# Kernel optimization log

Measured on AMD Instinct MI355X. Metric: run time of the kernel, lower is better.

The kernel has to match this reference:

```python
import jax, jax.numpy as jnp
import numpy as np

R = 65  # num_relations


def rgcn_conv(x, edge_index, edge_type, W, root, bias):
    """PyG RGCNConv with per-relation mean aggregation.
    Aggregate-then-transform (linearity lets us swap the order):
      mean_r[n] = mean over edges e with type r, dst(e)=n of x[src(e)]
      out = sum_r mean_r @ W_r + x @ root + bias
    """
    N = x.shape[0]
    src, dst = edge_index[0], edge_index[1]
    seg = edge_type * N + dst  # composite (relation, dst) segment id
    sums = jax.ops.segment_sum(x[src], seg, num_segments=R * N)
    sums = sums.reshape(R, N, -1)  # [R, N, F]
    cnt = jax.ops.segment_sum(jnp.ones(src.shape, x.dtype), seg, num_segments=R * N)
    cnt = cnt.reshape(R, N, 1)
    mean = sums / jnp.maximum(cnt, 1.0)
    return jnp.einsum('rni,rio->no', mean, W) + x @ root + bias


def setup_inputs() -> dict:
    key = jax.random.key(0)
    ks = jax.random.split(key, 20)
    N, E, F_in, H, M = 8000, 192000, 64, 256, 64
    B = 128
    inp = {
        'x': jax.random.normal(ks[0], (N, F_in), jnp.float32),
        'edge_index': jax.random.randint(ks[1], (2, E), 0, N),
        'edge_type': jax.random.randint(ks[2], (E,), 0, R),
        'batch': jnp.sort(jax.random.randint(ks[3], (N,), 0, B)),
    }
    def glorot(k, shape):
        fan = shape[-2] + shape[-1]
        return jax.random.normal(k, shape, jnp.float32) * jnp.sqrt(2.0 / fan)
    inp['W1'] = glorot(ks[4], (R, F_in, H)); inp['root1'] = glorot(ks[5], (F_in, H)); inp['b1'] = jnp.zeros((H,), jnp.float32)
    inp['W2'] = glorot(ks[6], (R, H, H));   inp['root2'] = glorot(ks[7], (H, H));   inp['b2'] = jnp.zeros((H,), jnp.float32)
    inp['W3'] = glorot(ks[8], (R, H, H));   inp['root3'] = glorot(ks[9], (H, H));   inp['b3'] = jnp.zeros((H,), jnp.float32)
    inp['ws_w'] = glorot(ks[10], (H, 1));    inp['ws_b'] = jnp.zeros((1,), jnp.float32)
    inp['m_w1'] = glorot(ks[11], (H, M)); inp['m_b1'] = jnp.zeros((M,), jnp.float32)
    inp['m_w2'] = glorot(ks[12], (M, M)); inp['m_b2'] = jnp.zeros((M,), jnp.float32)
    inp['m_w3'] = glorot(ks[13], (M, 1)); inp['m_b3'] = jnp.zeros((1,), jnp.float32)
    return inp


def reference(x, edge_index, edge_type, batch,
              W1, root1, b1, W2, root2, b2, W3, root3, b3,
              ws_w, ws_b, m_w1, m_b1, m_w2, m_b2, m_w3, m_b3):
    B = 128  # number of graphs in the batch
    h = jax.nn.relu(rgcn_conv(x, edge_index, edge_type, W1, root1, b1))
    h = jax.nn.relu(rgcn_conv(h, edge_index, edge_type, W2, root2, b2))
    h = jax.nn.relu(rgcn_conv(h, edge_index, edge_type, W3, root3, b3))
    # WeightedSum pooling: sigmoid gate per node, scatter-sum per graph
    w = jax.nn.sigmoid(h @ ws_w + ws_b)            # [N, 1]
    pooled = jax.ops.segment_sum(w * h, batch, num_segments=B)  # [B, H]
    # MLP head
    m = jax.nn.relu(pooled @ m_w1 + m_b1)
    m = jax.nn.relu(m @ m_w2 + m_b2)
    return m @ m_w3 + m_b3                          # [B, 1]
```

## Files before the change

### kernel.cpp

```cpp
#include <hip/hip_runtime.h>

#define NNODES 8000
#define NEDGES 192000
#define NREL   65
#define RP     66
#define HDIM   256
#define FDIM   64
#define NGRAPH 128
#define MDIM   64
#define TILE_M 64
#define MAXT   3456
#define EPTOT  (NEDGES + NNODES)

typedef _Float16 half8 __attribute__((ext_vector_type(8)));
typedef _Float16 half4 __attribute__((ext_vector_type(4)));
typedef float    f32x4 __attribute__((ext_vector_type(4)));
typedef unsigned int u32x4 __attribute__((ext_vector_type(4)));


__global__ void count_kernel(const int* __restrict__ ei, const int* __restrict__ et,
                             int* __restrict__ cnt_rn, int* __restrict__ type_cnt,
                             int* __restrict__ ddeg) {
    __shared__ int lbin[NREL];
    int tid = threadIdx.x;
    if (tid < NREL) lbin[tid] = 0;
    __syncthreads();
    int e = blockIdx.x * 256 + tid;
    if (e < NEDGES) {
        int t = et[e];
        int d = ei[NEDGES + e];
        atomicAdd(&lbin[t], 1);
        atomicAdd(&cnt_rn[t * NNODES + d], 1);
        atomicAdd(&ddeg[d], 1);
    }
    __syncthreads();
    if (tid < NREL && lbin[tid] > 0) atomicAdd(&type_cnt[tid], lbin[tid]);
}

__global__ void scan_tiles_kernel(const int* __restrict__ type_cnt, int* __restrict__ type_off,
                                  int* __restrict__ tile_rel, int* __restrict__ tile_start,
                                  int* __restrict__ tile_nrows) {
    __shared__ int s_off[RP + 1];
    __shared__ int s_toff[RP + 1];
    if (threadIdx.x == 0) {
        int off = 0, toff = 0;
        for (int r = 0; r < RP; r++) {
            int c = (r < NREL) ? type_cnt[r] : NNODES;
            s_off[r] = off; s_toff[r] = toff;
            off += c; toff += (c + TILE_M - 1) / TILE_M;
        }
        s_off[RP] = off; s_toff[RP] = toff;
        type_off[RP] = off;
    }
    __syncthreads();
    int r = threadIdx.x;
    if (r < RP) {
        type_off[r] = s_off[r];
        int c = s_off[r + 1] - s_off[r];
        int nt = (c + TILE_M - 1) / TILE_M;
        for (int i = 0; i < nt; i++) {
            int idx = s_toff[r] + i;
            tile_rel[idx]   = r;
            tile_start[idx] = s_off[r] + i * TILE_M;
            tile_nrows[idx] = min(TILE_M, c - i * TILE_M);
        }
    }
}

__global__ void dst_scan_kernel(const int* __restrict__ ddeg, int* __restrict__ dst_off) {
    __shared__ int part[256];
    int t = threadIdx.x;
    int base = t * 32;
    int s = 0;
    for (int i = 0; i < 32; i++) {
        int n = base + i;
        if (n < NNODES) s += ddeg[n] + 1;
    }
    part[t] = s;
    __syncthreads();
    if (t == 0) {
        int run = 0;
        for (int i = 0; i < 256; i++) { int tmp = part[i]; part[i] = run; run += tmp; }
        dst_off[NNODES] = run;
    }
    __syncthreads();
    int run = part[t];
    for (int i = 0; i < 32; i++) {
        int n = base + i;
        if (n < NNODES) { dst_off[n] = run; run += ddeg[n] + 1; }
    }
}

__global__ void scatter_kernel(const int* __restrict__ ei, const int* __restrict__ et,
                               const int* __restrict__ cnt_rn, const int* __restrict__ type_off,
                               int* __restrict__ type_cur,
                               const int* __restrict__ dst_off, int* __restrict__ dst_cur,
                               int* __restrict__ esrc, int* __restrict__ eq,
                               float* __restrict__ escale) {
    __shared__ int lbin[NREL];
    __shared__ int gbase[NREL];
    int tid = threadIdx.x;
    if (tid < NREL) lbin[tid] = 0;
    __syncthreads();
    int i = blockIdx.x * 256 + tid;
    int t = 0, lrank = 0;
    bool is_edge = (i < NEDGES);
    if (is_edge) {
        t = et[i];
        lrank = atomicAdd(&lbin[t], 1);
    }
    __syncthreads();
    if (tid < NREL && lbin[tid] > 0) gbase[tid] = atomicAdd(&type_cur[tid], lbin[tid]);
    __syncthreads();
    if (is_edge) {
        int d = ei[NEDGES + i];
        int p = type_off[t] + gbase[t] + lrank;
        int q = dst_off[d] + atomicAdd(&dst_cur[d], 1);
        esrc[p] = ei[i];
        eq[p] = q;
        escale[p] = 1.0f / (float)cnt_rn[t * NNODES + d];
    } else if (i < EPTOT) {
        int n = i - NEDGES;
        int p = NEDGES + n;
        int q = dst_off[n] + atomicAdd(&dst_cur[n], 1);
        esrc[p] = n; eq[p] = q; escale[p] = 1.0f;
    }
}

__global__ void convW_kernel(const float* __restrict__ W, const float* __restrict__ root,
                             _Float16* __restrict__ Wt, int K) {
    int r = blockIdx.x, k0 = blockIdx.y * 32, n0 = blockIdx.z * 32;
    const float* src = (r < NREL) ? (W + (size_t)r * K * HDIM) : root;
    __shared__ float tile[32][33];
    int tj = threadIdx.x & 31, ti = threadIdx.x >> 5;
    #pragma unroll
    for (int s = 0; s < 4; s++) {
        int i = ti + s * 8;
        tile[i][tj] = src[(size_t)(k0 + i) * HDIM + n0 + tj];
    }
    __syncthreads();
    #pragma unroll
    for (int s = 0; s < 4; s++) {
        int i = ti + s * 8;
        Wt[((size_t)r * HDIM + (n0 + i)) * K + k0 + tj] = (_Float16)tile[tj][i];
    }
}

__global__ void conv_x_kernel(const float* __restrict__ x, _Float16* __restrict__ x16) {
    int i = blockIdx.x * 256 + threadIdx.x;
    if (i < NNODES * FDIM) x16[i] = (_Float16)x[i];
}

template <int K>
__global__ __launch_bounds__(256)
void edge_gemm_kernel(const _Float16* __restrict__ hin, const _Float16* __restrict__ Wt,
                      const int* __restrict__ esrc, const int* __restrict__ eq,
                      const float* __restrict__ escale,
                      const int* __restrict__ tile_rel, const int* __restrict__ tile_start,
                      const int* __restrict__ tile_nrows,
                      _Float16* __restrict__ Y) {
    int bid  = blockIdx.x;
    int tile = (bid & 7) * (MAXT / 8) + (bid >> 3);

    int nr = tile_nrows[tile];
    if (nr == 0) return;
    int r  = tile_rel[tile];
    int ts = tile_start[tile];

    constexpr int KH  = (K > 128) ? 128 : K;
    constexpr int LK  = KH + 8;
    constexpr int SO  = HDIM + 8;
    constexpr int AEL = TILE_M * LK;
    constexpr int OEL = 32 * SO;
    constexpr int EL  = (AEL > OEL) ? AEL : OEL;
    __shared__ _Float16 sbuf[EL];
    __shared__ int   sq[TILE_M];
    __shared__ float sscale[TILE_M];

    int tid = threadIdx.x;
    if (tid < TILE_M) {
        if (tid < nr) { sq[tid] = eq[ts + tid]; sscale[tid] = escale[ts + tid]; }
        else          { sq[tid] = 0;            sscale[tid] = 0.f; }
    }

    int lane = tid & 63, w = tid >> 6;
    int lm = lane & 15, quad = lane >> 4;
    f32x4 acc[4][4] = {};
    const _Float16* Bbase = Wt + ((size_t)r * HDIM + w * 64 + lm) * K + quad * 8;
    const _Float16* Abase = sbuf + lm * LK + quad * 8;

    constexpr int CPR = KH / 8;
    for (int kh = 0; kh < K; kh += KH) {
        for (int idx = tid; idx < TILE_M * CPR; idx += 256) {
            int row = idx / CPR, c = idx % CPR;
            u32x4 v = {0, 0, 0, 0};
            if (row < nr) {
                int src = esrc[ts + row];
                v = *(const u32x4*)(hin + (size_t)src * K + kh + c * 8);
            }
            *(u32x4*)&sbuf[row * LK + c * 8] = v;
        }
        __syncthreads();

        for (int kk = 0; kk < KH; kk += 32) {
            half8 a[4], b[4];
            #pragma unroll
            for (int mt = 0; mt < 4; mt++)
                a[mt] = *(const half8*)(Abase + mt * 16 * LK + kk);
            #pragma unroll
            for (int nt = 0; nt < 4; nt++)
                b[nt] = *(const half8*)(Bbase + nt * 16 * K + kh + kk);
            #pragma unroll
            for (int mt = 0; mt < 4; mt++)
                #pragma unroll
                for (int nt = 0; nt < 4; nt++)
                    acc[mt][nt] = __builtin_amdgcn_mfma_f32_16x16x32_f16(a[mt], b[nt], acc[mt][nt], 0, 0, 0);
        }
        __syncthreads();
    }

    #pragma unroll
    for (int h = 0; h < 2; h++) {
        #pragma unroll
        for (int mh = 0; mh < 2; mh++) {
            int mt = h * 2 + mh;
            #pragma unroll
            for (int rr = 0; rr < 4; rr++) {
                int row  = mt * 16 + quad * 4 + rr;
                int lrow = row - h * 32;
                float s = sscale[row];
                #pragma unroll
                for (int nt = 0; nt < 4; nt++) {
                    int col = w * 64 + nt * 16 + lm;
                    sbuf[lrow * SO + col] = (_Float16)(acc[mt][nt][rr] * s);
                }
            }
        }
        __syncthreads();
        for (int idx = tid; idx < 32 * 32; idx += 256) {
            int lrow = idx >> 5, seg = idx & 31;
            int row = h * 32 + lrow;
            if (row < nr) {
                u32x4 v = *(const u32x4*)&sbuf[lrow * SO + seg * 8];
                __builtin_nontemporal_store(v, (u32x4*)(Y + (size_t)sq[row] * HDIM + seg * 8));
            }
        }
        if (h == 0) __syncthreads();
    }
}

__global__ __launch_bounds__(256)
void reduce_kernel(const _Float16* __restrict__ Y, const int* __restrict__ dst_off,
                   const float* __restrict__ bias, _Float16* __restrict__ hout) {
    int n = blockIdx.x;
    int start = dst_off[n], end = dst_off[n + 1];
    int t = threadIdx.x;
    int c = t & 31;
    int r = t >> 5;
    float acc[8] = {0, 0, 0, 0, 0, 0, 0, 0};
    for (int j = start + r; j < end; j += 8) {
        u32x4 u = __builtin_nontemporal_load((const u32x4*)(Y + (size_t)j * HDIM + c * 8));
        half8 v = *(half8*)&u;
        #pragma unroll
        for (int k = 0; k < 8; k++) acc[k] += (float)v[k];
    }
    __shared__ float red[8][32][8];
    #pragma unroll
    for (int k = 0; k < 8; k++) red[r][c][k] = acc[k];
    __syncthreads();
    if (t < 32) {
        float a[8];
        #pragma unroll
        for (int k = 0; k < 8; k++) a[k] = red[0][t][k];
        for (int rr = 1; rr < 8; rr++)
            #pragma unroll
            for (int k = 0; k < 8; k++) a[k] += red[rr][t][k];
        half8 o;
        #pragma unroll
        for (int k = 0; k < 8; k++) {
            float v = a[k] + bias[t * 8 + k];
            o[k] = (_Float16)(v > 0.f ? v : 0.f);
        }
        *(half8*)(hout + (size_t)n * HDIM + t * 8) = o;
    }
}


__global__ void gate_kernel(const _Float16* __restrict__ h, const float* __restrict__ ws_w,
                            const float* __restrict__ ws_b, float* __restrict__ gate) {
    int node = blockIdx.x * 4 + (threadIdx.x >> 6);
    int lane = threadIdx.x & 63;
    half4 v = *(const half4*)(h + (size_t)node * HDIM + lane * 4);
    float s = 0.f;
    #pragma unroll
    for (int k = 0; k < 4; k++) s += (float)v[k] * ws_w[lane * 4 + k];
    for (int o = 32; o > 0; o >>= 1) s += __shfl_down(s, o, 64);
    if (lane == 0) gate[node] = 1.f / (1.f + __expf(-(s + ws_b[0])));
}

__global__ void pool_kernel(const _Float16* __restrict__ h, const float* __restrict__ gate,
                            const int* __restrict__ batch, float* __restrict__ pooled) {
    int g = blockIdx.x, t = threadIdx.x;
    int a = 0, b = NNODES;
    while (a < b) { int m = (a + b) >> 1; if (batch[m] < g) a = m + 1; else b = m; }
    int lo = a;
    b = NNODES;
    while (a < b) { int m = (a + b) >> 1; if (batch[m] < g + 1) a = m + 1; else b = m; }
    int hi = a;
    float acc = 0.f;
    for (int n = lo; n < hi; n++)
        acc += gate[n] * (float)h[(size_t)n * HDIM + t];
    pooled[(size_t)g * HDIM + t] = acc;
}

__global__ void head_kernel(const float* __restrict__ pooled,
                            const float* __restrict__ w1, const float* __restrict__ b1,
                            const float* __restrict__ w2, const float* __restrict__ b2,
                            const float* __restrict__ w3, const float* __restrict__ b3,
                            float* __restrict__ out) {
    int b = blockIdx.x, tid = threadIdx.x;
    __shared__ float sp[HDIM];
    __shared__ float m1[MDIM];
    __shared__ float m2[MDIM];
    for (int i = tid; i < HDIM; i += 64) sp[i] = pooled[(size_t)b * HDIM + i];
    __syncthreads();
    float a = b1[tid];
    for (int i = 0; i < HDIM; i++) a += sp[i] * w1[i * MDIM + tid];
    m1[tid] = a > 0.f ? a : 0.f;
    __syncthreads();
    float c = b2[tid];
    for (int i = 0; i < MDIM; i++) c += m1[i] * w2[i * MDIM + tid];
    m2[tid] = c > 0.f ? c : 0.f;
    __syncthreads();
    float p = m2[tid] * w3[tid];
    for (int o = 32; o > 0; o >>= 1) p += __shfl_down(p, o, 64);
    if (tid == 0) out[b] = p + b3[0];
}


extern "C" void kernel_launch(void* const* d_in, const int* in_sizes, int n_in,
                              void* d_out, int out_size, void* d_ws, size_t ws_size,
                              hipStream_t stream) {
    const float* x     = (const float*)d_in[0];
    const int*   ei    = (const int*)d_in[1];
    const int*   et    = (const int*)d_in[2];
    const int*   batch = (const int*)d_in[3];
    const float* W1    = (const float*)d_in[4];
    const float* root1 = (const float*)d_in[5];
    const float* b1    = (const float*)d_in[6];
    const float* W2    = (const float*)d_in[7];
    const float* root2 = (const float*)d_in[8];
    const float* b2    = (const float*)d_in[9];
    const float* W3    = (const float*)d_in[10];
    const float* root3 = (const float*)d_in[11];
    const float* b3    = (const float*)d_in[12];
    const float* ws_w  = (const float*)d_in[13];
    const float* ws_b  = (const float*)d_in[14];
    const float* m_w1  = (const float*)d_in[15];
    const float* m_b1  = (const float*)d_in[16];
    const float* m_w2  = (const float*)d_in[17];
    const float* m_b2  = (const float*)d_in[18];
    const float* m_w3  = (const float*)d_in[19];
    const float* m_b3  = (const float*)d_in[20];
    float* out = (float*)d_out;

    char* ws = (char*)d_ws;
    size_t o = 0;
    auto take = [&](size_t bytes) { size_t r = o; o = (o + bytes + 255) & ~(size_t)255; return r; };

    size_t o_cnt_rn = take((size_t)NREL * NNODES * 4);
    size_t o_tcnt   = take(RP * 4);
    size_t o_tcur   = take(RP * 4);
    size_t o_toff   = take((RP + 1) * 4);
    size_t o_ddeg   = take((size_t)NNODES * 4);
    size_t o_dcur   = take((size_t)NNODES * 4);
    size_t o_doff   = take((size_t)(NNODES + 1) * 4);
    size_t o_esrc   = take((size_t)EPTOT * 4);
    size_t o_eq     = take((size_t)EPTOT * 4);
    size_t o_escale = take((size_t)EPTOT * 4);
    size_t o_trel   = take(MAXT * 4);
    size_t o_tstart = take(MAXT * 4);
    size_t o_tnrows = take(MAXT * 4);
    size_t o_wt1    = take((size_t)RP * HDIM * FDIM * 2);
    size_t o_wt2    = take((size_t)RP * HDIM * HDIM * 2);
    size_t o_wt3    = take((size_t)RP * HDIM * HDIM * 2);
    size_t o_x16    = take((size_t)NNODES * FDIM * 2);
    size_t o_h16    = take((size_t)NNODES * HDIM * 2);
    size_t o_gate   = take((size_t)NNODES * 4);
    size_t o_pool   = take((size_t)NGRAPH * HDIM * 4);
    size_t o_y16    = take((size_t)EPTOT * HDIM * 2);

    int*      cnt_rn   = (int*)(ws + o_cnt_rn);
    int*      type_cnt = (int*)(ws + o_tcnt);
    int*      type_cur = (int*)(ws + o_tcur);
    int*      type_off = (int*)(ws + o_toff);
    int*      ddeg     = (int*)(ws + o_ddeg);
    int*      dst_cur  = (int*)(ws + o_dcur);
    int*      dst_off  = (int*)(ws + o_doff);
    int*      esrc     = (int*)(ws + o_esrc);
    int*      eq       = (int*)(ws + o_eq);
    float*    escale   = (float*)(ws + o_escale);
    int*      trel     = (int*)(ws + o_trel);
    int*      tstart   = (int*)(ws + o_tstart);
    int*      tnrows   = (int*)(ws + o_tnrows);
    _Float16* Wt1      = (_Float16*)(ws + o_wt1);
    _Float16* Wt2      = (_Float16*)(ws + o_wt2);
    _Float16* Wt3      = (_Float16*)(ws + o_wt3);
    _Float16* x16      = (_Float16*)(ws + o_x16);
    _Float16* h16      = (_Float16*)(ws + o_h16);
    float*    gate     = (float*)(ws + o_gate);
    float*    pooled   = (float*)(ws + o_pool);
    _Float16* Y16      = (_Float16*)(ws + o_y16);

    hipMemsetAsync(ws + o_cnt_rn, 0, o_toff - o_cnt_rn, stream);
    hipMemsetAsync(ws + o_ddeg, 0, o_doff - o_ddeg, stream);
    hipMemsetAsync(ws + o_tnrows, 0, MAXT * 4, stream);

    count_kernel<<<(NEDGES + 255) / 256, 256, 0, stream>>>(ei, et, cnt_rn, type_cnt, ddeg);
    scan_tiles_kernel<<<1, 128, 0, stream>>>(type_cnt, type_off, trel, tstart, tnrows);
    dst_scan_kernel<<<1, 256, 0, stream>>>(ddeg, dst_off);
    scatter_kernel<<<(EPTOT + 255) / 256, 256, 0, stream>>>(ei, et, cnt_rn, type_off, type_cur,
                                                            dst_off, dst_cur, esrc, eq, escale);

    convW_kernel<<<dim3(RP, FDIM / 32, HDIM / 32), 256, 0, stream>>>(W1, root1, Wt1, FDIM);
    convW_kernel<<<dim3(RP, HDIM / 32, HDIM / 32), 256, 0, stream>>>(W2, root2, Wt2, HDIM);
    convW_kernel<<<dim3(RP, HDIM / 32, HDIM / 32), 256, 0, stream>>>(W3, root3, Wt3, HDIM);
    conv_x_kernel<<<(NNODES * FDIM + 255) / 256, 256, 0, stream>>>(x, x16);

    edge_gemm_kernel<FDIM><<<MAXT, 256, 0, stream>>>(x16, Wt1, esrc, eq, escale,
                                                     trel, tstart, tnrows, Y16);
    reduce_kernel<<<NNODES, 256, 0, stream>>>(Y16, dst_off, b1, h16);

    edge_gemm_kernel<HDIM><<<MAXT, 256, 0, stream>>>(h16, Wt2, esrc, eq, escale,
                                                     trel, tstart, tnrows, Y16);
    reduce_kernel<<<NNODES, 256, 0, stream>>>(Y16, dst_off, b2, h16);

    edge_gemm_kernel<HDIM><<<MAXT, 256, 0, stream>>>(h16, Wt3, esrc, eq, escale,
                                                     trel, tstart, tnrows, Y16);
    reduce_kernel<<<NNODES, 256, 0, stream>>>(Y16, dst_off, b3, h16);

    gate_kernel<<<NNODES / 4, 256, 0, stream>>>(h16, ws_w, ws_b, gate);
    pool_kernel<<<NGRAPH, 256, 0, stream>>>(h16, gate, batch, pooled);
    head_kernel<<<NGRAPH, 64, 0, stream>>>(pooled, m_w1, m_b1, m_w2, m_b2, m_w3, m_b3, out);

    (void)in_sizes; (void)n_in; (void)out_size; (void)ws_size;
}
```

Baseline: 503.9 us.

## Split edge GEMM output columns across two blocks and use wave-per-node reduce

The edge GEMM now launches twice as many blocks, each computing half of the 256 output columns. This halves the accumulator registers and lets launch bounds request 8 blocks per CU for higher occupancy. The cost is that the gathered A rows are loaded twice, once per half. The tile index mapping is also reordered into chunks of 384, and the reduce kernel changes from a block per node with a shared-memory reduction to a wavefront per node combined with shuffles.

Result: no change. 511.3 us (+1.5%).

```diff
diff --git a/kernel.cpp b/kernel.cpp
--- a/kernel.cpp
+++ b/kernel.cpp
@@ -152,15 +152,19 @@
 }
 
 template <int K>
-__global__ __launch_bounds__(256)
+__global__ __launch_bounds__(256, 8)
 void edge_gemm_kernel(const _Float16* __restrict__ hin, const _Float16* __restrict__ Wt,
                       const int* __restrict__ esrc, const int* __restrict__ eq,
                       const float* __restrict__ escale,
                       const int* __restrict__ tile_rel, const int* __restrict__ tile_start,
                       const int* __restrict__ tile_nrows,
                       _Float16* __restrict__ Y) {
-    int bid  = blockIdx.x;
-    int tile = (bid & 7) * (MAXT / 8) + (bid >> 3);
+    int bid = blockIdx.x;
+    int ch  = (bid >= MAXT) ? 1 : 0;
+    int t   = bid - ch * MAXT;
+    int x = t & 7, i = t >> 3;
+    int c = i / 48, j = i % 48;
+    int tile = c * 384 + x * 48 + j;
 
     int nr = tile_nrows[tile];
     if (nr == 0) return;
@@ -169,9 +173,9 @@
 
     constexpr int KH  = (K > 128) ? 128 : K;
     constexpr int LK  = KH + 8;
-    constexpr int SO  = HDIM + 8;
+    constexpr int SO  = 136;
     constexpr int AEL = TILE_M * LK;
-    constexpr int OEL = 32 * SO;
+    constexpr int OEL = TILE_M * SO;
     constexpr int EL  = (AEL > OEL) ? AEL : OEL;
     __shared__ _Float16 sbuf[EL];
     __shared__ int   sq[TILE_M];
@@ -185,103 +189,82 @@
 
     int lane = tid & 63, w = tid >> 6;
     int lm = lane & 15, quad = lane >> 4;
-    f32x4 acc[4][4] = {};
-    const _Float16* Bbase = Wt + ((size_t)r * HDIM + w * 64 + lm) * K + quad * 8;
+    f32x4 acc[4][2] = {};
+    const _Float16* Bbase = Wt + ((size_t)r * HDIM + ch * 128 + w * 32 + lm) * K + quad * 8;
     const _Float16* Abase = sbuf + lm * LK + quad * 8;
 
     constexpr int CPR = KH / 8;
     for (int kh = 0; kh < K; kh += KH) {
         for (int idx = tid; idx < TILE_M * CPR; idx += 256) {
-            int row = idx / CPR, c = idx % CPR;
+            int row = idx / CPR, cc = idx % CPR;
             u32x4 v = {0, 0, 0, 0};
             if (row < nr) {
                 int src = esrc[ts + row];
-                v = *(const u32x4*)(hin + (size_t)src * K + kh + c * 8);
+                v = *(const u32x4*)(hin + (size_t)src * K + kh + cc * 8);
             }
-            *(u32x4*)&sbuf[row * LK + c * 8] = v;
+            *(u32x4*)&sbuf[row * LK + cc * 8] = v;
         }
         __syncthreads();
 
         for (int kk = 0; kk < KH; kk += 32) {
-            half8 a[4], b[4];
+            half8 b0 = *(const half8*)(Bbase + kh + kk);
+            half8 b1 = *(const half8*)(Bbase + 16 * K + kh + kk);
             #pragma unroll
-            for (int mt = 0; mt < 4; mt++)
-                a[mt] = *(const half8*)(Abase + mt * 16 * LK + kk);
+            for (int mt = 0; mt < 4; mt++) {
+                half8 a = *(const half8*)(Abase + mt * 16 * LK + kk);
+                acc[mt][0] = __builtin_amdgcn_mfma_f32_16x16x32_f16(a, b0, acc[mt][0], 0, 0, 0);
+                acc[mt][1] = __builtin_amdgcn_mfma_f32_16x16x32_f16(a, b1, acc[mt][1], 0, 0, 0);
+            }
+        }
+        __syncthreads();
+    }
+
+    #pragma unroll
+    for (int mt = 0; mt < 4; mt++) {
+        #pragma unroll
+        for (int rr = 0; rr < 4; rr++) {
+            int row = mt * 16 + quad * 4 + rr;
+            float s = sscale[row];
             #pragma unroll
-            for (int nt = 0; nt < 4; nt++)
-                b[nt] = *(const half8*)(Bbase + nt * 16 * K + kh + kk);
-            #pragma unroll
-            for (int mt = 0; mt < 4; mt++)
-                #pragma unroll
-                for (int nt = 0; nt < 4; nt++)
-                    acc[mt][nt] = __builtin_amdgcn_mfma_f32_16x16x32_f16(a[mt], b[nt], acc[mt][nt], 0, 0, 0);
-        }
-        __syncthreads();
-    }
-
-    #pragma unroll
-    for (int h = 0; h < 2; h++) {
-        #pragma unroll
-        for (int mh = 0; mh < 2; mh++) {
-            int mt = h * 2 + mh;
-            #pragma unroll
-            for (int rr = 0; rr < 4; rr++) {
-                int row  = mt * 16 + quad * 4 + rr;
-                int lrow = row - h * 32;
-                float s = sscale[row];
-                #pragma unroll
-                for (int nt = 0; nt < 4; nt++) {
-                    int col = w * 64 + nt * 16 + lm;
-                    sbuf[lrow * SO + col] = (_Float16)(acc[mt][nt][rr] * s);
-                }
-            }
-        }
-        __syncthreads();
-        for (int idx = tid; idx < 32 * 32; idx += 256) {
-            int lrow = idx >> 5, seg = idx & 31;
-            int row = h * 32 + lrow;
-            if (row < nr) {
-                u32x4 v = *(const u32x4*)&sbuf[lrow * SO + seg * 8];
-                __builtin_nontemporal_store(v, (u32x4*)(Y + (size_t)sq[row] * HDIM + seg * 8));
-            }
-        }
-        if (h == 0) __syncthreads();
+            for (int nt = 0; nt < 2; nt++)
+                sbuf[row * SO + w * 32 + nt * 16 + lm] = (_Float16)(acc[mt][nt][rr] * s);
+        }
+    }
+    __syncthreads();
+    for (int idx = tid; idx < TILE_M * 16; idx += 256) {
+        int row = idx >> 4, seg = idx & 15;
+        if (row < nr) {
+            u32x4 v = *(const u32x4*)&sbuf[row * SO + seg * 8];
+            __builtin_nontemporal_store(v, (u32x4*)(Y + (size_t)sq[row] * HDIM + ch * 128 + seg * 8));
+        }
     }
 }
 
 __global__ __launch_bounds__(256)
 void reduce_kernel(const _Float16* __restrict__ Y, const int* __restrict__ dst_off,
                    const float* __restrict__ bias, _Float16* __restrict__ hout) {
-    int n = blockIdx.x;
-    int start = dst_off[n], end = dst_off[n + 1];
-    int t = threadIdx.x;
-    int c = t & 31;
-    int r = t >> 5;
+    int node = blockIdx.x * 4 + (threadIdx.x >> 6);
+    int lane = threadIdx.x & 63;
+    int start = dst_off[node], end = dst_off[node + 1];
+    int c = lane & 31;
+    int r = lane >> 5;
     float acc[8] = {0, 0, 0, 0, 0, 0, 0, 0};
-    for (int j = start + r; j < end; j += 8) {
-        u32x4 u = __builtin_nontemporal_load((const u32x4*)(Y + (size_t)j * HDIM + c * 8));
+    for (int jj = start + r; jj < end; jj += 2) {
+        u32x4 u = __builtin_nontemporal_load((const u32x4*)(Y + (size_t)jj * HDIM + c * 8));
         half8 v = *(half8*)&u;
         #pragma unroll
         for (int k = 0; k < 8; k++) acc[k] += (float)v[k];
     }
-    __shared__ float red[8][32][8];
     #pragma unroll
-    for (int k = 0; k < 8; k++) red[r][c][k] = acc[k];
-    __syncthreads();
-    if (t < 32) {
-        float a[8];
-        #pragma unroll
-        for (int k = 0; k < 8; k++) a[k] = red[0][t][k];
-        for (int rr = 1; rr < 8; rr++)
-            #pragma unroll
-            for (int k = 0; k < 8; k++) a[k] += red[rr][t][k];
+    for (int k = 0; k < 8; k++) acc[k] += __shfl_down(acc[k], 32, 64);
+    if (lane < 32) {
         half8 o;
         #pragma unroll
         for (int k = 0; k < 8; k++) {
-            float v = a[k] + bias[t * 8 + k];
+            float v = acc[k] + bias[c * 8 + k];
             o[k] = (_Float16)(v > 0.f ? v : 0.f);
         }
-        *(half8*)(hout + (size_t)n * HDIM + t * 8) = o;
+        *(half8*)(hout + (size_t)node * HDIM + c * 8) = o;
     }
 }
 
@@ -427,17 +410,17 @@
     convW_kernel<<<dim3(RP, HDIM / 32, HDIM / 32), 256, 0, stream>>>(W3, root3, Wt3, HDIM);
     conv_x_kernel<<<(NNODES * FDIM + 255) / 256, 256, 0, stream>>>(x, x16);
 
-    edge_gemm_kernel<FDIM><<<MAXT, 256, 0, stream>>>(x16, Wt1, esrc, eq, escale,
-                                                     trel, tstart, tnrows, Y16);
-    reduce_kernel<<<NNODES, 256, 0, stream>>>(Y16, dst_off, b1, h16);
-
-    edge_gemm_kernel<HDIM><<<MAXT, 256, 0, stream>>>(h16, Wt2, esrc, eq, escale,
-                                                     trel, tstart, tnrows, Y16);
-    reduce_kernel<<<NNODES, 256, 0, stream>>>(Y16, dst_off, b2, h16);
-
-    edge_gemm_kernel<HDIM><<<MAXT, 256, 0, stream>>>(h16, Wt3, esrc, eq, escale,
-                                                     trel, tstart, tnrows, Y16);
-    reduce_kernel<<<NNODES, 256, 0, stream>>>(Y16, dst_off, b3, h16);
+    edge_gemm_kernel<FDIM><<<2 * MAXT, 256, 0, stream>>>(x16, Wt1, esrc, eq, escale,
+                                                         trel, tstart, tnrows, Y16);
+    reduce_kernel<<<NNODES / 4, 256, 0, stream>>>(Y16, dst_off, b1, h16);
+
+    edge_gemm_kernel<HDIM><<<2 * MAXT, 256, 0, stream>>>(h16, Wt2, esrc, eq, escale,
+                                                         trel, tstart, tnrows, Y16);
+    reduce_kernel<<<NNODES / 4, 256, 0, stream>>>(Y16, dst_off, b2, h16);
+
+    edge_gemm_kernel<HDIM><<<2 * MAXT, 256, 0, stream>>>(h16, Wt3, esrc, eq, escale,
+                                                         trel, tstart, tnrows, Y16);
+    reduce_kernel<<<NNODES / 4, 256, 0, stream>>>(Y16, dst_off, b3, h16);
 
     gate_kernel<<<NNODES / 4, 256, 0, stream>>>(h16, ws_w, ws_b, gate);
     pool_kernel<<<NGRAPH, 256, 0, stream>>>(h16, gate, batch, pooled);
```
